# Kernel tuning notes

Measured on AMD Instinct MI355X. Metric: run time of the kernel, lower is better.

Reference implementation:

```python
import jax, jax.numpy as jnp
import numpy as np

B, NA, LAT, HID, AF, L = 512, 58, 64, 128, 10, 2
N = B * NA
E = N * 16


def silu(x):
    return x * jax.nn.sigmoid(x)


def setup_inputs() -> dict:
    key = jax.random.key(0)
    ks = list(jax.random.split(key, 32))

    def p(k, shape, fan_in):
        return jax.random.normal(k, shape, jnp.float32) / np.sqrt(fan_in)

    inp = {
        "z": jax.random.normal(ks[0], (B, LAT), jnp.float32),
        "atom_types": jax.random.uniform(ks[1], (N, AF), jnp.float32),
        "edge_index": jax.random.randint(ks[2], (2, E), 0, N, jnp.int64),
        "init_coords": jax.random.normal(ks[3], (NA, 3), jnp.float32) * 0.1,
        "latent_w": p(ks[4], (LAT, HID), LAT), "latent_b": jnp.zeros((HID,), jnp.float32),
        "atom_w": p(ks[5], (AF, HID), AF), "atom_b": jnp.zeros((HID,), jnp.float32),
        # per-layer stacked params (leading dim = num_layers)
        "edge_w1": p(ks[6], (L, 2 * HID + 1, HID), 2 * HID + 1), "edge_b1": jnp.zeros((L, HID), jnp.float32),
        "edge_w2": p(ks[7], (L, HID, HID), HID), "edge_b2": jnp.zeros((L, HID), jnp.float32),
        "node_w1": p(ks[8], (L, 2 * HID, HID), 2 * HID), "node_b1": jnp.zeros((L, HID), jnp.float32),
        "node_w2": p(ks[9], (L, HID, HID), HID), "node_b2": jnp.zeros((L, HID), jnp.float32),
        "coord_w1": p(ks[10], (L, HID, HID), HID), "coord_b1": jnp.zeros((L, HID), jnp.float32),
        "coord_w2": p(ks[11], (L, HID, 1), HID),  # no bias
        "ln_g": jnp.ones((L, HID), jnp.float32), "ln_b": jnp.zeros((L, HID), jnp.float32),
        "head_w1": p(ks[12], (HID, HID // 2), HID), "head_b1": jnp.zeros((HID // 2,), jnp.float32),
        "head_w2": p(ks[13], (HID // 2, 3), HID // 2), "head_b2": jnp.zeros((3,), jnp.float32),
    }
    return inp


def _layer(h, pos, row, col, ew1, eb1, ew2, eb2, nw1, nb1, nw2, nb2, cw1, cb1, cw2, lg, lb):
    n = h.shape[0]
    xi, xj = h[row], h[col]                      # [E,HID] gathers
    rel = pos[row] - pos[col]                    # [E,3]
    d2 = jnp.clip(jnp.sum(rel * rel, axis=-1, keepdims=True), 1e-6, 1e6)
    ef = jnp.concatenate([xi, xj, d2], axis=-1)  # [E,2H+1]
    m = silu(silu(ef @ ew1 + eb1) @ ew2 + eb2)   # edge MLP messages [E,HID]
    agg = jax.ops.segment_sum(m, row, num_segments=n)
    hn = silu(jnp.concatenate([h, agg], axis=-1) @ nw1 + nb1) @ nw2 + nb2
    mu = jnp.mean(hn, axis=-1, keepdims=True)
    var = jnp.mean((hn - mu) ** 2, axis=-1, keepdims=True)
    hn = (hn - mu) * jax.lax.rsqrt(var + 1e-5) * lg + lb
    cw = jnp.clip(silu(m @ cw1 + cb1) @ cw2, -1.0, 1.0)  # [E,1]
    upd = jax.ops.segment_sum(cw * rel, row, num_segments=n)  # [N,3]
    deg = jax.ops.segment_sum(jnp.ones((row.shape[0],), pos.dtype), row, num_segments=n)[:, None]
    pos_new = pos + upd / (deg + 1e-6)
    return hn, pos_new


def reference(z, atom_types, edge_index, init_coords, latent_w, latent_b, atom_w, atom_b,
              edge_w1, edge_b1, edge_w2, edge_b2, node_w1, node_b1, node_w2, node_b2,
              coord_w1, coord_b1, coord_w2, ln_g, ln_b, head_w1, head_b1, head_w2, head_b2):
    b = z.shape[0]
    na = init_coords.shape[0]
    n = b * na
    h = z @ latent_w + latent_b                              # [B,HID]
    h = jnp.broadcast_to(h[:, None, :], (b, na, h.shape[-1])).reshape(n, -1)
    h = h + (atom_types @ atom_w + atom_b)
    pos = jnp.broadcast_to(init_coords[None], (b, na, 3)).reshape(n, 3)
    row, col = edge_index[0], edge_index[1]
    for l in range(edge_w1.shape[0]):
        h, pos = _layer(h, pos, row, col,
                        edge_w1[l], edge_b1[l], edge_w2[l], edge_b2[l],
                        node_w1[l], node_b1[l], node_w2[l], node_b2[l],
                        coord_w1[l], coord_b1[l], coord_w2[l], ln_g[l], ln_b[l])
    delta = silu(h @ head_w1 + head_b1) @ head_w2 + head_b2
    return pos + delta
```

## Files before the change

### kernel.cpp

```cpp
#include <hip/hip_runtime.h>
#include <hip/hip_bf16.h>

#define BB 512
#define NA 58
#define LAT 64
#define HID 128
#define AF 10
#define NL 2
#define NN (BB*NA)
#define NE (NN*16)
#define ET 64
#define NTILE (NE/ET)
#define PBLK 768

typedef __attribute__((ext_vector_type(8))) short s8;
typedef __attribute__((ext_vector_type(4))) float f4;

struct CvtDesc {
    const void* src[24];
    float*      dst[24];
    int         len[24];
};

struct PackJobs {
    const float* src[10];
    short*       dst[10];
    int          K[10];
    int          mode[10];
};

__device__ __forceinline__ float siluf(float x) {
    return x * __builtin_amdgcn_rcpf(1.0f + __expf(-x));
}

__device__ __forceinline__ short f2b(float x) {
    __hip_bfloat16 b = __float2bfloat16(x);
    return *(short*)&b;
}

__device__ __forceinline__ float b2f(short s) {
    return __uint_as_float(((unsigned int)(unsigned short)s) << 16);
}

__global__ void k_detect(const unsigned short* __restrict__ z16,
                         const unsigned int* __restrict__ e32,
                         int* __restrict__ flags) {
    __shared__ int sbf, si64;
    if (threadIdx.x == 0) { sbf = 0; si64 = 0; }
    __syncthreads();
    int c1 = 0, c2 = 0;
    for (int i = threadIdx.x; i < 1024; i += 256) {
        unsigned short v = z16[2*i];
        int e = (v >> 7) & 0xFF;
        if (e >= 100 && e <= 140) c1++;
        if (e32[2*i + 1] == 0u) c2++;
    }
    atomicAdd(&sbf, c1);
    atomicAdd(&si64, c2);
    __syncthreads();
    if (threadIdx.x == 0) {
        flags[0] = (sbf  > 600) ? 1 : 0;
        flags[1] = (si64 > 600) ? 1 : 0;
    }
}

__global__ void k_convert(CvtDesc d, const int* __restrict__ flags) {
    int a = blockIdx.y;
    int i = blockIdx.x * blockDim.x + threadIdx.x;
    int n = d.len[a];
    if (i >= n) return;
    if (flags[0]) {
        d.dst[a][i] = __bfloat162float(((const __hip_bfloat16*)d.src[a])[i]);
    } else {
        d.dst[a][i] = ((const float*)d.src[a])[i];
    }
}

__global__ void k_packall(PackJobs pj) {
    int j = blockIdx.y;
    int idx = blockIdx.x * 256 + threadIdx.x;
    const float* w = pj.src[j];
    short* o = pj.dst[j];
    if (pj.mode[j] == 0) {
        int K = pj.K[j];
        if (idx >= 128*K) return;
        int jj = idx & 7;
        int l  = (idx >> 3) & 63;
        int rest = idx >> 9;
        int KC = K >> 5;
        int kc = rest % KC;
        int nt = rest / KC;
        int n = nt*16 + (l & 15);
        int k = kc*32 + (l >> 4)*8 + jj;
        o[idx] = f2b(w[k*128 + n]);
    } else {
        if (idx >= 32768) return;
        int jj = idx & 7;
        int l  = (idx >> 3) & 63;
        int rest = idx >> 9;
        int kc = rest & 3;
        int nt = rest >> 2;
        int n = nt*16 + (l & 15);
        int k = kc*32 + (l >> 4)*8 + jj;
        float v = (n < 128) ? w[k*128 + n] : w[(128 + k)*128 + (n - 128)];
        o[idx] = f2b(v);
    }
}

__global__ void k_hist(const int* __restrict__ eidx, const int* __restrict__ flags,
                       int* __restrict__ cnt) {
    int e = blockIdx.x * 256 + threadIdx.x;
    if (e >= NE) return;
    int is64 = flags[1];
    int r = eidx[is64 ? 2*(long)e : (long)e];
    atomicAdd(&cnt[r], 1);
}

__global__ __launch_bounds__(1024) void k_scan(const int* __restrict__ cnt,
                                               int* __restrict__ rowStart,
                                               int* __restrict__ cursor) {
    __shared__ int part[1024];
    int t = threadIdx.x;
    int base = t * 29;
    int loc[29];
    int s = 0;
    #pragma unroll
    for (int i = 0; i < 29; ++i) { loc[i] = s; s += cnt[base + i]; }
    part[t] = s;
    __syncthreads();
    for (int d = 1; d < 1024; d <<= 1) {
        int v = (t >= d) ? part[t - d] : 0;
        __syncthreads();
        part[t] += v;
        __syncthreads();
    }
    int pre = (t == 0) ? 0 : part[t - 1];
    #pragma unroll
    for (int i = 0; i < 29; ++i) {
        int v = pre + loc[i];
        rowStart[base + i] = v;
        cursor[base + i] = v;
    }
    if (t == 1023) rowStart[NN] = pre + s;
}

__global__ void k_scatter(const int* __restrict__ eidx, const int* __restrict__ flags,
                          int* __restrict__ cursor,
                          int* __restrict__ rS, int* __restrict__ cS) {
    int e = blockIdx.x * 256 + threadIdx.x;
    if (e >= NE) return;
    int is64 = flags[1];
    long ge = e, gc = (long)e + NE;
    int r = eidx[is64 ? 2*ge : ge];
    int c = eidx[is64 ? 2*gc : gc];
    int p = atomicAdd(&cursor[r], 1);
    rS[p] = r; cS[p] = c;
}

__global__ void k_hz(const float* __restrict__ z, const float* __restrict__ lw,
                     const float* __restrict__ lb, float* __restrict__ hz) {
    __shared__ float zs[LAT];
    int b = blockIdx.x;
    int c = threadIdx.x;
    if (c < LAT) zs[c] = z[b*LAT + c];
    __syncthreads();
    float acc = lb[c];
    #pragma unroll
    for (int k = 0; k < LAT; ++k) acc += zs[k] * lw[k*HID + c];
    hz[b*HID + c] = acc;
}

__global__ __launch_bounds__(256) void k_init3(
    const float* __restrict__ hz, const float* __restrict__ at,
    const float* __restrict__ aw, const float* __restrict__ ab,
    const float* __restrict__ ic,
    float* __restrict__ pos, short* __restrict__ hb,
    const short* __restrict__ wcat0, const float* __restrict__ b10,
    short* __restrict__ H1, float* __restrict__ agg, float* __restrict__ upd)
{
    __shared__ short x[64][136];
    __shared__ float awS[AF][HID];
    __shared__ float atS[64][AF+2];
    const int tid = threadIdx.x;
    const int n0 = blockIdx.x * 64;

    for (int i = tid; i < AF*HID; i += 256) awS[i/HID][i%HID] = aw[i];
    for (int i = tid; i < 64*AF; i += 256)
        atS[i/AF][i%AF] = at[(long)(n0 + i/AF)*AF + i%AF];
    __syncthreads();

    #pragma unroll
    for (int it = 0; it < 32; ++it) {
        int idx = it*256 + tid;
        int r = idx >> 7, c = idx & 127;
        int n = n0 + r;
        int bb = n / NA;
        float v = hz[bb*HID + c] + ab[c];
        #pragma unroll
        for (int f = 0; f < AF; ++f) v += atS[r][f]*awS[f][c];
        short s = f2b(v);
        x[r][c] = s;
        hb[(long)n*HID + c] = s;
    }
    if (tid < 192) {
        int i = tid/3, d = tid - i*3;
        int n = n0 + i;
        pos[n*3 + d] = ic[(n % NA)*3 + d];
        upd[n*3 + d] = 0.f;
    }
    {
        f4* a4 = (f4*)(agg + (long)n0*HID);
        for (int j = tid; j < 64*HID/4; j += 256) a4[j] = (f4)0.f;
    }
    __syncthreads();

    const int l = tid & 63, w = tid >> 6;
    const int l16 = l & 15, quad = l >> 4;
    f4 acc[4][4];
    #pragma unroll
    for (int mt = 0; mt < 4; ++mt)
        #pragma unroll
        for (int nt4 = 0; nt4 < 4; ++nt4) acc[mt][nt4] = (f4)0.f;
    #pragma unroll
    for (int kc = 0; kc < 4; ++kc) {
        s8 a[4];
        #pragma unroll
        for (int mt = 0; mt < 4; ++mt)
            a[mt] = *(const s8*)&x[mt*16 + l16][kc*32 + quad*8];
        #pragma unroll
        for (int nt4 = 0; nt4 < 4; ++nt4) {
            int nt = w*4 + nt4;
            s8 b = *(const s8*)(wcat0 + (((size_t)nt*4 + kc)*64 + l)*8);
            #pragma unroll
            for (int mt = 0; mt < 4; ++mt)
                acc[mt][nt4] = __builtin_amdgcn_mfma_f32_16x16x32_bf16(a[mt], b, acc[mt][nt4], 0, 0, 0);
        }
    }
    #pragma unroll
    for (int nt4 = 0; nt4 < 4; ++nt4) {
        int col = (w*4 + nt4)*16 + l16;
        float bias = (col < 128) ? b10[col] : 0.f;
        #pragma unroll
        for (int mt = 0; mt < 4; ++mt)
            #pragma unroll
            for (int i = 0; i < 4; ++i) {
                int row = mt*16 + quad*4 + i;
                H1[(long)(n0 + row)*256 + col] = f2b(acc[mt][nt4][i] + bias);
            }
    }
}

__global__ __launch_bounds__(256, 3) void k_edge8(
    const short* __restrict__ H1,
    const int* __restrict__ rS, const int* __restrict__ cS,
    const float* __restrict__ pos,
    const float* __restrict__ w1c,
    const short* __restrict__ w2p, const float* __restrict__ b2,
    const short* __restrict__ c1p, const float* __restrict__ cb1,
    const float* __restrict__ cw2,
    float* __restrict__ agg, float* __restrict__ upd)
{
    __shared__ short t1[2][ET][136];
    __shared__ short mm[ET][136];
    __shared__ int   rIs[2][ET], cIs[2][ET];
    __shared__ float sred[ET];

    const int tid = threadIdx.x;
    const int l = tid & 63, w = tid >> 6;
    const int l16 = l & 15, quad = l >> 4;
    const int c0 = (2*w)*16 + l16, c1c = (2*w+1)*16 + l16;
    const int half = tid >> 7, ch = tid & 127;
    const int q = tid & 15;
    const int esub = tid >> 4;

    float wv[8];
    #pragma unroll
    for (int j = 0; j < 8; ++j) wv[j] = w1c[q*8 + j];

    s8 w2f[8], c1f[8];
    #pragma unroll
    for (int kc = 0; kc < 4; ++kc) {
        w2f[kc]     = *(const s8*)(w2p + (((size_t)(2*w)*4 + kc)*64 + l)*8);
        w2f[4 + kc] = *(const s8*)(w2p + (((size_t)(2*w+1)*4 + kc)*64 + l)*8);
        c1f[kc]     = *(const s8*)(c1p + (((size_t)(2*w)*4 + kc)*64 + l)*8);
        c1f[4 + kc] = *(const s8*)(c1p + (((size_t)(2*w+1)*4 + kc)*64 + l)*8);
    }
    const float bia2_0 = b2[c0],  bia2_1 = b2[c1c];
    const float biac_0 = cb1[c0], biac_1 = cb1[c1c];
    const float cw0    = cw2[c0], cw1v   = cw2[c1c];

    int   pri[4], pci[4];
    float pd2[4];
    auto PREIDX = [&](int T) {
        long eb = (long)T * ET;
        #pragma unroll
        for (int it = 0; it < 4; ++it) {
            int e = esub + 16*it;
            int r = rS[eb + e], c = cS[eb + e];
            pri[it] = r; pci[it] = c;
            float rx = pos[r*3+0] - pos[c*3+0];
            float ry = pos[r*3+1] - pos[c*3+1];
            float rz = pos[r*3+2] - pos[c*3+2];
            pd2[it] = fminf(fmaxf(rx*rx + ry*ry + rz*rz, 1e-6f), 1e6f);
        }
    };

    int T = blockIdx.x;
    PREIDX(T);
    #pragma unroll
    for (int it = 0; it < 4; ++it) {
        s8 va = *(const s8*)(H1 + (long)pri[it]*256 + q*8);
        s8 vb = *(const s8*)(H1 + (long)pci[it]*256 + 128 + q*8);
        float d2 = pd2[it];
        s8 o;
        #pragma unroll
        for (int j = 0; j < 8; ++j)
            o[j] = f2b(siluf(b2f(va[j]) + b2f(vb[j]) + d2*wv[j]));
        *(s8*)&t1[0][esub + 16*it][q*8] = o;
    }
    if (q == 0) {
        #pragma unroll
        for (int it = 0; it < 4; ++it) {
            rIs[0][esub + 16*it] = pri[it];
            cIs[0][esub + 16*it] = pci[it];
        }
    }
    if (tid < ET) sred[tid] = 0.f;
    int Tn = T + PBLK;
    if (Tn < NTILE) PREIDX(Tn);
    __syncthreads();

    int b = 0;
    while (true) {
        const bool hasNext = (Tn < NTILE);

        {
            f4 acc[4][2];
            #pragma unroll
            for (int mt = 0; mt < 4; ++mt) { acc[mt][0] = (f4)0.f; acc[mt][1] = (f4)0.f; }
            #pragma unroll
            for (int it = 0; it < 4; ++it) {
                s8 va, vb;
                if (hasNext) {
                    va = *(const s8*)(H1 + (long)pri[it]*256 + q*8);
                    vb = *(const s8*)(H1 + (long)pci[it]*256 + 128 + q*8);
                }
                #pragma unroll
                for (int mt = 0; mt < 4; ++mt) {
                    s8 a = *(const s8*)&t1[b][mt*16 + l16][it*32 + quad*8];
                    acc[mt][0] = __builtin_amdgcn_mfma_f32_16x16x32_bf16(a, w2f[it],     acc[mt][0], 0, 0, 0);
                    acc[mt][1] = __builtin_amdgcn_mfma_f32_16x16x32_bf16(a, w2f[4 + it], acc[mt][1], 0, 0, 0);
                }
                if (hasNext) {
                    float d2 = pd2[it];
                    s8 o;
                    #pragma unroll
                    for (int j = 0; j < 8; ++j)
                        o[j] = f2b(siluf(b2f(va[j]) + b2f(vb[j]) + d2*wv[j]));
                    *(s8*)&t1[b^1][esub + 16*it][q*8] = o;
                }
            }
            if (hasNext && q == 0) {
                #pragma unroll
                for (int it = 0; it < 4; ++it) {
                    rIs[b^1][esub + 16*it] = pri[it];
                    cIs[b^1][esub + 16*it] = pci[it];
                }
            }
            #pragma unroll
            for (int mt = 0; mt < 4; ++mt) {
                #pragma unroll
                for (int i = 0; i < 4; ++i) {
                    int row = mt*16 + quad*4 + i;
                    mm[row][c0]  = f2b(siluf(acc[mt][0][i] + bia2_0));
                    mm[row][c1c] = f2b(siluf(acc[mt][1][i] + bia2_1));
                }
            }
        }
        __syncthreads();

        {
            f4 acc[4][2];
            #pragma unroll
            for (int mt = 0; mt < 4; ++mt) { acc[mt][0] = (f4)0.f; acc[mt][1] = (f4)0.f; }
            #pragma unroll
            for (int kc = 0; kc < 4; ++kc) {
                #pragma unroll
                for (int mt = 0; mt < 4; ++mt) {
                    s8 a = *(const s8*)&mm[mt*16 + l16][kc*32 + quad*8];
                    acc[mt][0] = __builtin_amdgcn_mfma_f32_16x16x32_bf16(a, c1f[kc],     acc[mt][0], 0, 0, 0);
                    acc[mt][1] = __builtin_amdgcn_mfma_f32_16x16x32_bf16(a, c1f[4 + kc], acc[mt][1], 0, 0, 0);
                }
            }
            #pragma unroll
            for (int mt = 0; mt < 4; ++mt) {
                #pragma unroll
                for (int i = 0; i < 4; ++i) {
                    float p = siluf(acc[mt][0][i] + biac_0) * cw0
                            + siluf(acc[mt][1][i] + biac_1) * cw1v;
                    p += __shfl_xor(p, 1);
                    p += __shfl_xor(p, 2);
                    p += __shfl_xor(p, 4);
                    p += __shfl_xor(p, 8);
                    if (l16 == 0) {
                        int row = mt*16 + quad*4 + i;
                        atomicAdd(&sred[row], p);
                    }
                }
            }
        }
        {
            int e0 = half * 32;
            int cur = rIs[b][e0];
            float a = 0.f;
            #pragma unroll
            for (int e = e0; e < e0 + 32; ++e) {
                int r = rIs[b][e];
                if (r != cur) {
                    atomicAdd(&agg[(long)cur*HID + ch], a);
                    a = 0.f; cur = r;
                }
                a += b2f(mm[e][ch]);
            }
            atomicAdd(&agg[(long)cur*HID + ch], a);
        }
        int Tnn = Tn + PBLK;
        if (hasNext && Tnn < NTILE) PREIDX(Tnn);
        __syncthreads();

        if (tid < ET) {
            float cwv = fminf(fmaxf(sred[tid], -1.f), 1.f);
            sred[tid] = 0.f;
            int r = rIs[b][tid], c = cIs[b][tid];
            float rx = pos[r*3+0] - pos[c*3+0];
            float ry = pos[r*3+1] - pos[c*3+1];
            float rz = pos[r*3+2] - pos[c*3+2];
            atomicAdd(&upd[r*3+0], cwv*rx);
            atomicAdd(&upd[r*3+1], cwv*ry);
            atomicAdd(&upd[r*3+2], cwv*rz);
        }
        if (!hasNext) break;
        T = Tn; Tn = Tnn; b ^= 1;
    }
}

__global__ __launch_bounds__(256) void k_node_mfma(
    short* __restrict__ hb, float* __restrict__ agg,
    const short* __restrict__ w1p, const float* __restrict__ b1n,
    const short* __restrict__ w2p, const float* __restrict__ b2n,
    const float* __restrict__ lg, const float* __restrict__ lb,
    float* __restrict__ pos, float* __restrict__ upd,
    const int* __restrict__ rowStart,
    const short* __restrict__ wcatn, const float* __restrict__ b1next,
    short* __restrict__ H1)
{
    __shared__ short x[64][264];
    __shared__ short t1[64][144];
    __shared__ float mus[64], rstds[64];
    float (*hn)[132] = (float (*)[132])&x[0][0];

    const int tid = threadIdx.x;
    const int n0 = blockIdx.x * 64;

    #pragma unroll
    for (int it = 0; it < 4; ++it) {
        int idx = it*256 + tid;
        int e = idx >> 4, qq = idx & 15;
        *(int4*)&x[e][qq*8] = *(const int4*)(hb + (long)(n0+e)*HID + qq*8);
    }
    #pragma unroll
    for (int it = 0; it < 8; ++it) {
        int idx = it*256 + tid;
        int e = idx >> 5, qq = idx & 31;
        float4 v = *(const float4*)(agg + (long)(n0+e)*HID + qq*4);
        short4 sv;
        sv.x = f2b(v.x); sv.y = f2b(v.y); sv.z = f2b(v.z); sv.w = f2b(v.w);
        *(short4*)&x[e][128 + qq*4] = sv;
    }
    __syncthreads();

    {
        f4* a4 = (f4*)(agg + (long)n0*HID);
        for (int j = tid; j < 64*HID/4; j += 256) a4[j] = (f4)0.f;
    }

    const int l = tid & 63, w = tid >> 6;
    const int l16 = l & 15, quad = l >> 4;
    const int nt0 = 2*w, nt1 = 2*w + 1;
    const int c0 = nt0*16 + l16, c1c = nt1*16 + l16;

    {
        f4 acc[4][2];
        #pragma unroll
        for (int mt = 0; mt < 4; ++mt) { acc[mt][0] = (f4)0.f; acc[mt][1] = (f4)0.f; }
        #pragma unroll
        for (int kc = 0; kc < 8; ++kc) {
            s8 b0  = *(const s8*)(w1p + (((size_t)nt0*8 + kc)*64 + l)*8);
            s8 b1f = *(const s8*)(w1p + (((size_t)nt1*8 + kc)*64 + l)*8);
            #pragma unroll
            for (int mt = 0; mt < 4; ++mt) {
                s8 a = *(const s8*)&x[mt*16 + l16][kc*32 + quad*8];
                acc[mt][0] = __builtin_amdgcn_mfma_f32_16x16x32_bf16(a, b0,  acc[mt][0], 0, 0, 0);
                acc[mt][1] = __builtin_amdgcn_mfma_f32_16x16x32_bf16(a, b1f, acc[mt][1], 0, 0, 0);
            }
        }
        float bia0 = b1n[c0], bia1 = b1n[c1c];
        #pragma unroll
        for (int mt = 0; mt < 4; ++mt) {
            #pragma unroll
            for (int i = 0; i < 4; ++i) {
                int row = mt*16 + quad*4 + i;
                t1[row][c0]  = f2b(siluf(acc[mt][0][i] + bia0));
                t1[row][c1c] = f2b(siluf(acc[mt][1][i] + bia1));
            }
        }
    }
    __syncthreads();

    {
        f4 acc[4][2];
        #pragma unroll
        for (int mt = 0; mt < 4; ++mt) { acc[mt][0] = (f4)0.f; acc[mt][1] = (f4)0.f; }
        #pragma unroll
        for (int kc = 0; kc < 4; ++kc) {
            s8 b0  = *(const s8*)(w2p + (((size_t)nt0*4 + kc)*64 + l)*8);
            s8 b1f = *(const s8*)(w2p + (((size_t)nt1*4 + kc)*64 + l)*8);
            #pragma unroll
            for (int mt = 0; mt < 4; ++mt) {
                s8 a = *(const s8*)&t1[mt*16 + l16][kc*32 + quad*8];
                acc[mt][0] = __builtin_amdgcn_mfma_f32_16x16x32_bf16(a, b0,  acc[mt][0], 0, 0, 0);
                acc[mt][1] = __builtin_amdgcn_mfma_f32_16x16x32_bf16(a, b1f, acc[mt][1], 0, 0, 0);
            }
        }
        float bia0 = b2n[c0], bia1 = b2n[c1c];
        __syncthreads();
        #pragma unroll
        for (int mt = 0; mt < 4; ++mt) {
            #pragma unroll
            for (int i = 0; i < 4; ++i) {
                int row = mt*16 + quad*4 + i;
                hn[row][c0]  = acc[mt][0][i] + bia0;
                hn[row][c1c] = acc[mt][1][i] + bia1;
            }
        }
    }
    __syncthreads();

    {
        int r = tid >> 2, part = tid & 3;
        float s = 0.f, qv = 0.f;
        #pragma unroll
        for (int j = 0; j < 32; ++j) {
            float v = hn[r][part + 4*j];
            s += v; qv += v*v;
        }
        s += __shfl_xor(s, 1); qv += __shfl_xor(qv, 1);
        s += __shfl_xor(s, 2); qv += __shfl_xor(qv, 2);
        if (part == 0) {
            float mu = s * (1.0f/HID);
            float var = qv * (1.0f/HID) - mu*mu;
            mus[r] = mu;
            rstds[r] = rsqrtf(var + 1e-5f);
        }
    }
    __syncthreads();

    #pragma unroll
    for (int it = 0; it < 32; ++it) {
        int idx = it*256 + tid;
        int r = idx >> 7, c = idx & 127;
        float v = (hn[r][c] - mus[r]) * rstds[r] * lg[c] + lb[c];
        short s = f2b(v);
        hb[(long)(n0 + r)*HID + c] = s;
        t1[r][c] = s;
    }
    if (tid < 192) {
        int i = tid / 3, d = tid - i*3;
        int n = n0 + i;
        float dg = (float)(rowStart[n+1] - rowStart[n]);
        pos[n*3+d] += upd[n*3+d] / (dg + 1e-6f);
        upd[n*3+d] = 0.f;
    }

    if (wcatn) {
        __syncthreads();
        f4 acc[4][4];
        #pragma unroll
        for (int mt = 0; mt < 4; ++mt)
            #pragma unroll
            for (int nt4 = 0; nt4 < 4; ++nt4) acc[mt][nt4] = (f4)0.f;
        #pragma unroll
        for (int kc = 0; kc < 4; ++kc) {
            s8 a[4];
            #pragma unroll
            for (int mt = 0; mt < 4; ++mt)
                a[mt] = *(const s8*)&t1[mt*16 + l16][kc*32 + quad*8];
            #pragma unroll
            for (int nt4 = 0; nt4 < 4; ++nt4) {
                int nt = w*4 + nt4;
                s8 b = *(const s8*)(wcatn + (((size_t)nt*4 + kc)*64 + l)*8);
                #pragma unroll
                for (int mt = 0; mt < 4; ++mt)
                    acc[mt][nt4] = __builtin_amdgcn_mfma_f32_16x16x32_bf16(a[mt], b, acc[mt][nt4], 0, 0, 0);
            }
        }
        #pragma unroll
        for (int nt4 = 0; nt4 < 4; ++nt4) {
            int col = (w*4 + nt4)*16 + l16;
            float bias = (col < 128) ? b1next[col] : 0.f;
            #pragma unroll
            for (int mt = 0; mt < 4; ++mt)
                #pragma unroll
                for (int i = 0; i < 4; ++i) {
                    int row = mt*16 + quad*4 + i;
                    H1[(long)(n0 + row)*256 + col] = f2b(acc[mt][nt4][i] + bias);
                }
        }
    }
}

__global__ void k_head(const short* __restrict__ hb, const float* __restrict__ pos,
                       const float* __restrict__ w1, const float* __restrict__ b1,
                       const float* __restrict__ w2, const float* __restrict__ b2,
                       void* __restrict__ out, const int* __restrict__ flags)
{
    __shared__ float hs[4][HID];
    __shared__ float t[4][64];
    const int tid = threadIdx.x;
    const int n0 = blockIdx.x * 4;
    for (int i = tid; i < 4*HID; i += 256)
        hs[i >> 7][i & 127] = b2f(hb[(long)n0*HID + i]);
    __syncthreads();
    const int s = tid >> 6, c = tid & 63;
    float acc = b1[c];
    for (int k4 = 0; k4 < 32; ++k4) {
        int k = k4*4;
        float wa = w1[(k+0)*64 + c];
        float wb = w1[(k+1)*64 + c];
        float wc = w1[(k+2)*64 + c];
        float wd = w1[(k+3)*64 + c];
        float4 v = *(const float4*)&hs[s][k];
        acc += v.x*wa + v.y*wb + v.z*wc + v.w*wd;
    }
    t[s][c] = siluf(acc);
    __syncthreads();
    if (c < 3) {
        float a2 = b2[c];
        #pragma unroll
        for (int k = 0; k < 64; ++k) a2 += t[s][k] * w2[k*3 + c];
        int n = n0 + s;
        float v = pos[n*3+c] + a2;
        if (flags[0]) ((__hip_bfloat16*)out)[n*3+c] = __float2bfloat16(v);
        else          ((float*)out)[n*3+c] = v;
    }
}

extern "C" void kernel_launch(void* const* d_in, const int* in_sizes, int n_in,
                              void* d_out, int out_size, void* d_ws, size_t ws_size,
                              hipStream_t stream)
{
    (void)in_sizes; (void)n_in; (void)out_size; (void)ws_size;

    int* flags = (int*)d_ws;
    float* base = (float*)d_ws;
    size_t off = 64;
    auto alloc = [&](size_t n) { float* p = base + off; off += (n + 63) & ~63ull; return p; };

    static const int aidx[24] = {0,1,3,4,5,6,7,8,9,10,11,12,13,14,15,16,17,18,19,20,21,22,23,24};
    static const int alen[24] = {
        BB*LAT, NN*AF, NA*3, LAT*HID, HID, AF*HID, HID,
        NL*257*HID, NL*HID, NL*HID*HID, NL*HID,
        NL*256*HID, NL*HID, NL*HID*HID, NL*HID,
        NL*HID*HID, NL*HID, NL*HID, NL*HID, NL*HID,
        HID*64, 64, 64*3, 3
    };
    CvtDesc cd;
    float* fp[24];
    for (int a = 0; a < 24; ++a) {
        fp[a] = alloc((size_t)alen[a]);
        cd.src[a] = d_in[aidx[a]];
        cd.dst[a] = fp[a];
        cd.len[a] = alen[a];
    }
    float* agg = alloc((size_t)NN*HID);
    float* hz  = alloc((size_t)BB*HID);
    float* pos = alloc((size_t)NN*3);
    float* upd = alloc((size_t)NN*3);
    short* hb  = (short*)alloc((size_t)NN*HID/2);
    short* H1  = (short*)alloc((size_t)NN*256/2);
    short* wcatp = (short*)alloc((size_t)NL*32768/2);
    short* w2p = (short*)alloc((size_t)NL*16384/2);
    short* c1p = (short*)alloc((size_t)NL*16384/2);
    short* nw1p = (short*)alloc((size_t)NL*32768/2);
    short* nw2p = (short*)alloc((size_t)NL*16384/2);
    int* cnt      = (int*)alloc((size_t)NN);
    int* rowStart = (int*)alloc((size_t)NN + 1);
    int* cursor   = (int*)alloc((size_t)NN);
    int* rS       = (int*)alloc((size_t)NE);
    int* cS       = (int*)alloc((size_t)NE);
    const int* eidx = (const int*)d_in[2];

    k_detect<<<1, 256, 0, stream>>>((const unsigned short*)d_in[0],
                                    (const unsigned int*)d_in[2], flags);
    k_convert<<<dim3((NN*AF + 255)/256, 24), 256, 0, stream>>>(cd, flags);

    PackJobs pj;
    for (int l = 0; l < NL; ++l) {
        int b5 = l*5;
        pj.src[b5+0] = fp[7]  + (size_t)l*257*HID; pj.dst[b5+0] = wcatp + (size_t)l*32768; pj.K[b5+0] = 256; pj.mode[b5+0] = 1;
        pj.src[b5+1] = fp[9]  + (size_t)l*HID*HID; pj.dst[b5+1] = w2p   + (size_t)l*16384; pj.K[b5+1] = 128; pj.mode[b5+1] = 0;
        pj.src[b5+2] = fp[15] + (size_t)l*HID*HID; pj.dst[b5+2] = c1p   + (size_t)l*16384; pj.K[b5+2] = 128; pj.mode[b5+2] = 0;
        pj.src[b5+3] = fp[11] + (size_t)l*256*HID; pj.dst[b5+3] = nw1p  + (size_t)l*32768; pj.K[b5+3] = 256; pj.mode[b5+3] = 0;
        pj.src[b5+4] = fp[13] + (size_t)l*HID*HID; pj.dst[b5+4] = nw2p  + (size_t)l*16384; pj.K[b5+4] = 128; pj.mode[b5+4] = 0;
    }
    k_packall<<<dim3(128, 10), 256, 0, stream>>>(pj);

    hipMemsetAsync(cnt, 0, (size_t)NN*sizeof(int), stream);
    k_hist<<<(NE + 255)/256, 256, 0, stream>>>(eidx, flags, cnt);
    k_scan<<<1, 1024, 0, stream>>>(cnt, rowStart, cursor);
    k_scatter<<<(NE + 255)/256, 256, 0, stream>>>(eidx, flags, cursor, rS, cS);

    k_hz<<<BB, HID, 0, stream>>>(fp[0], fp[3], fp[4], hz);
    k_init3<<<NN/64, 256, 0, stream>>>(hz, fp[1], fp[5], fp[6], fp[2], pos, hb,
                                       wcatp, fp[8], H1, agg, upd);

    for (int l = 0; l < NL; ++l) {
        k_edge8<<<PBLK, 256, 0, stream>>>(H1, rS, cS, pos,
            fp[7] + (size_t)l*257*HID + 256*HID,
            w2p + (size_t)l*16384, fp[10] + (size_t)l*HID,
            c1p + (size_t)l*16384, fp[16] + (size_t)l*HID,
            fp[17] + (size_t)l*HID,
            agg, upd);
        const short* wcatn = (l+1 < NL) ? (wcatp + (size_t)(l+1)*32768) : nullptr;
        const float* b1nx  = (l+1 < NL) ? (fp[8] + (size_t)(l+1)*HID) : fp[8];
        k_node_mfma<<<NN/64, 256, 0, stream>>>(hb, agg,
            nw1p + (size_t)l*32768, fp[12] + (size_t)l*HID,
            nw2p + (size_t)l*16384, fp[14] + (size_t)l*HID,
            fp[18] + (size_t)l*HID, fp[19] + (size_t)l*HID,
            pos, upd, rowStart, wcatn, b1nx, H1);
    }
    k_head<<<NN/4, 256, 0, stream>>>(hb, pos, fp[20], fp[21], fp[22], fp[23],
                                     d_out, flags);
}
```

Before: 647.4 us.

## Restructure edge kernel to per-wave 16-edge tiles and fuse head into node kernel

The edge kernel changes from block-level 64-edge tiles with double-buffered shared memory and block barriers to independent per-wave 16-edge tiles. Each wave builds its MFMA A operand directly in registers and reads the packed weights from global/L1 on every tile instead of keeping them resident in registers. This removes __syncthreads and shared-memory staging of the first activation, but it reloads weight fragments per tile and issues more atomics with shorter segment runs. Separately, the output head MLP is packed to bf16 and fused into the last node kernel via MFMA, which removes the k_head launch and the re-read of h.

```diff
diff --git a/kernel.cpp b/kernel.cpp
--- a/kernel.cpp
+++ b/kernel.cpp
@@ -9,8 +9,7 @@
 #define NL 2
 #define NN (BB*NA)
 #define NE (NN*16)
-#define ET 64
-#define NTILE (NE/ET)
+#define NWT (NE/16)
 #define PBLK 768
 
 typedef __attribute__((ext_vector_type(8))) short s8;
@@ -23,10 +22,10 @@
 };
 
 struct PackJobs {
-    const float* src[10];
-    short*       dst[10];
-    int          K[10];
-    int          mode[10];
+    const float* src[11];
+    short*       dst[11];
+    int          K[11];
+    int          mode[11];
 };
 
 __device__ __forceinline__ float siluf(float x) {
@@ -81,7 +80,8 @@
     int idx = blockIdx.x * 256 + threadIdx.x;
     const float* w = pj.src[j];
     short* o = pj.dst[j];
-    if (pj.mode[j] == 0) {
+    int mode = pj.mode[j];
+    if (mode == 0) {
         int K = pj.K[j];
         if (idx >= 128*K) return;
         int jj = idx & 7;
@@ -93,7 +93,7 @@
         int n = nt*16 + (l & 15);
         int k = kc*32 + (l >> 4)*8 + jj;
         o[idx] = f2b(w[k*128 + n]);
-    } else {
+    } else if (mode == 1) {
         if (idx >= 32768) return;
         int jj = idx & 7;
         int l  = (idx >> 3) & 63;
@@ -104,6 +104,16 @@
         int k = kc*32 + (l >> 4)*8 + jj;
         float v = (n < 128) ? w[k*128 + n] : w[(128 + k)*128 + (n - 128)];
         o[idx] = f2b(v);
+    } else {
+        if (idx >= 8192) return;
+        int jj = idx & 7;
+        int l  = (idx >> 3) & 63;
+        int rest = idx >> 9;
+        int kc = rest & 3;
+        int nt = rest >> 2;
+        int n = nt*16 + (l & 15);
+        int k = kc*32 + (l >> 4)*8 + jj;
+        o[idx] = f2b(w[k*64 + n]);
     }
 }
 
@@ -250,7 +260,7 @@
     }
 }
 
-__global__ __launch_bounds__(256, 3) void k_edge8(
+__global__ __launch_bounds__(256, 3) void k_edge9(
     const short* __restrict__ H1,
     const int* __restrict__ rS, const int* __restrict__ cS,
     const float* __restrict__ pos,
@@ -260,187 +270,116 @@
     const float* __restrict__ cw2,
     float* __restrict__ agg, float* __restrict__ upd)
 {
-    __shared__ short t1[2][ET][136];
-    __shared__ short mm[ET][136];
-    __shared__ int   rIs[2][ET], cIs[2][ET];
-    __shared__ float sred[ET];
+    __shared__ short msc[4][16][136];
+    __shared__ float cwS[4][16];
 
     const int tid = threadIdx.x;
-    const int l = tid & 63, w = tid >> 6;
+    const int w = tid >> 6, l = tid & 63;
     const int l16 = l & 15, quad = l >> 4;
-    const int c0 = (2*w)*16 + l16, c1c = (2*w+1)*16 + l16;
-    const int half = tid >> 7, ch = tid & 127;
-    const int q = tid & 15;
-    const int esub = tid >> 4;
-
-    float wv[8];
-    #pragma unroll
-    for (int j = 0; j < 8; ++j) wv[j] = w1c[q*8 + j];
-
-    s8 w2f[8], c1f[8];
-    #pragma unroll
-    for (int kc = 0; kc < 4; ++kc) {
-        w2f[kc]     = *(const s8*)(w2p + (((size_t)(2*w)*4 + kc)*64 + l)*8);
-        w2f[4 + kc] = *(const s8*)(w2p + (((size_t)(2*w+1)*4 + kc)*64 + l)*8);
-        c1f[kc]     = *(const s8*)(c1p + (((size_t)(2*w)*4 + kc)*64 + l)*8);
-        c1f[4 + kc] = *(const s8*)(c1p + (((size_t)(2*w+1)*4 + kc)*64 + l)*8);
-    }
-    const float bia2_0 = b2[c0],  bia2_1 = b2[c1c];
-    const float biac_0 = cb1[c0], biac_1 = cb1[c1c];
-    const float cw0    = cw2[c0], cw1v   = cw2[c1c];
-
-    int   pri[4], pci[4];
-    float pd2[4];
-    auto PREIDX = [&](int T) {
-        long eb = (long)T * ET;
-        #pragma unroll
-        for (int it = 0; it < 4; ++it) {
-            int e = esub + 16*it;
-            int r = rS[eb + e], c = cS[eb + e];
-            pri[it] = r; pci[it] = c;
-            float rx = pos[r*3+0] - pos[c*3+0];
-            float ry = pos[r*3+1] - pos[c*3+1];
-            float rz = pos[r*3+2] - pos[c*3+2];
-            pd2[it] = fminf(fmaxf(rx*rx + ry*ry + rz*rz, 1e-6f), 1e6f);
-        }
-    };
-
-    int T = blockIdx.x;
-    PREIDX(T);
-    #pragma unroll
-    for (int it = 0; it < 4; ++it) {
-        s8 va = *(const s8*)(H1 + (long)pri[it]*256 + q*8);
-        s8 vb = *(const s8*)(H1 + (long)pci[it]*256 + 128 + q*8);
-        float d2 = pd2[it];
-        s8 o;
-        #pragma unroll
-        for (int j = 0; j < 8; ++j)
-            o[j] = f2b(siluf(b2f(va[j]) + b2f(vb[j]) + d2*wv[j]));
-        *(s8*)&t1[0][esub + 16*it][q*8] = o;
-    }
-    if (q == 0) {
-        #pragma unroll
-        for (int it = 0; it < 4; ++it) {
-            rIs[0][esub + 16*it] = pri[it];
-            cIs[0][esub + 16*it] = pci[it];
-        }
-    }
-    if (tid < ET) sred[tid] = 0.f;
-    int Tn = T + PBLK;
-    if (Tn < NTILE) PREIDX(Tn);
-    __syncthreads();
-
-    int b = 0;
-    while (true) {
-        const bool hasNext = (Tn < NTILE);
+
+    float b2l[8], cbl[8], cwl[8];
+    #pragma unroll
+    for (int nt = 0; nt < 8; ++nt) {
+        b2l[nt] = b2[nt*16 + l16];
+        cbl[nt] = cb1[nt*16 + l16];
+        cwl[nt] = cw2[nt*16 + l16];
+    }
+
+    for (int wt = blockIdx.x*4 + w; wt < NWT; wt += PBLK*4) {
+        const long eb = (long)wt * 16;
+
+        int r = rS[eb + l16], c = cS[eb + l16];
+        float rx = pos[r*3+0] - pos[c*3+0];
+        float ry = pos[r*3+1] - pos[c*3+1];
+        float rz = pos[r*3+2] - pos[c*3+2];
+        float d2 = fminf(fmaxf(rx*rx + ry*ry + rz*rz, 1e-6f), 1e6f);
+
+        s8 a[4];
+        #pragma unroll
+        for (int kc = 0; kc < 4; ++kc) {
+            s8 va = *(const s8*)(H1 + (long)r*256 + kc*32 + quad*8);
+            s8 vb = *(const s8*)(H1 + (long)c*256 + 128 + kc*32 + quad*8);
+            f4 w0 = *(const f4*)(w1c + kc*32 + quad*8);
+            f4 w1v = *(const f4*)(w1c + kc*32 + quad*8 + 4);
+            s8 o;
+            #pragma unroll
+            for (int j = 0; j < 8; ++j) {
+                float wvj = (j < 4) ? w0[j & 3] : w1v[j & 3];
+                o[j] = f2b(siluf(b2f(va[j]) + b2f(vb[j]) + d2*wvj));
+            }
+            a[kc] = o;
+        }
+
+        #pragma unroll
+        for (int nt = 0; nt < 8; ++nt) {
+            f4 acc = (f4)0.f;
+            #pragma unroll
+            for (int kc = 0; kc < 4; ++kc) {
+                s8 b = *(const s8*)(w2p + (((size_t)nt*4 + kc)*64 + l)*8);
+                acc = __builtin_amdgcn_mfma_f32_16x16x32_bf16(a[kc], b, acc, 0, 0, 0);
+            }
+            int col = nt*16 + l16;
+            #pragma unroll
+            for (int i = 0; i < 4; ++i)
+                msc[w][quad*4 + i][col] = f2b(siluf(acc[i] + b2l[nt]));
+        }
+
+        s8 ma[4];
+        #pragma unroll
+        for (int kc = 0; kc < 4; ++kc)
+            ma[kc] = *(const s8*)&msc[w][l16][kc*32 + quad*8];
+
+        float accr[4] = {0.f, 0.f, 0.f, 0.f};
+        #pragma unroll
+        for (int nt = 0; nt < 8; ++nt) {
+            f4 acc = (f4)0.f;
+            #pragma unroll
+            for (int kc = 0; kc < 4; ++kc) {
+                s8 b = *(const s8*)(c1p + (((size_t)nt*4 + kc)*64 + l)*8);
+                acc = __builtin_amdgcn_mfma_f32_16x16x32_bf16(ma[kc], b, acc, 0, 0, 0);
+            }
+            #pragma unroll
+            for (int i = 0; i < 4; ++i)
+                accr[i] += siluf(acc[i] + cbl[nt]) * cwl[nt];
+        }
+        #pragma unroll
+        for (int i = 0; i < 4; ++i) {
+            float p = accr[i];
+            p += __shfl_xor(p, 1);
+            p += __shfl_xor(p, 2);
+            p += __shfl_xor(p, 4);
+            p += __shfl_xor(p, 8);
+            if (l16 == 0) cwS[w][quad*4 + i] = fminf(fmaxf(p, -1.f), 1.f);
+        }
 
         {
-            f4 acc[4][2];
-            #pragma unroll
-            for (int mt = 0; mt < 4; ++mt) { acc[mt][0] = (f4)0.f; acc[mt][1] = (f4)0.f; }
-            #pragma unroll
-            for (int it = 0; it < 4; ++it) {
-                s8 va, vb;
-                if (hasNext) {
-                    va = *(const s8*)(H1 + (long)pri[it]*256 + q*8);
-                    vb = *(const s8*)(H1 + (long)pci[it]*256 + 128 + q*8);
+            float s0 = 0.f, s1 = 0.f;
+            int cur = rS[eb];
+            #pragma unroll
+            for (int k = 0; k < 16; ++k) {
+                int rr = rS[eb + k];
+                if (rr != cur) {
+                    atomicAdd(&agg[(long)cur*HID + l],      s0);
+                    atomicAdd(&agg[(long)cur*HID + l + 64], s1);
+                    s0 = 0.f; s1 = 0.f; cur = rr;
                 }
-                #pragma unroll
-                for (int mt = 0; mt < 4; ++mt) {
-                    s8 a = *(const s8*)&t1[b][mt*16 + l16][it*32 + quad*8];
-                    acc[mt][0] = __builtin_amdgcn_mfma_f32_16x16x32_bf16(a, w2f[it],     acc[mt][0], 0, 0, 0);
-                    acc[mt][1] = __builtin_amdgcn_mfma_f32_16x16x32_bf16(a, w2f[4 + it], acc[mt][1], 0, 0, 0);
-                }
-                if (hasNext) {
-                    float d2 = pd2[it];
-                    s8 o;
-                    #pragma unroll
-                    for (int j = 0; j < 8; ++j)
-                        o[j] = f2b(siluf(b2f(va[j]) + b2f(vb[j]) + d2*wv[j]));
-                    *(s8*)&t1[b^1][esub + 16*it][q*8] = o;
-                }
-            }
-            if (hasNext && q == 0) {
-                #pragma unroll
-                for (int it = 0; it < 4; ++it) {
-                    rIs[b^1][esub + 16*it] = pri[it];
-                    cIs[b^1][esub + 16*it] = pci[it];
-                }
-            }
-            #pragma unroll
-            for (int mt = 0; mt < 4; ++mt) {
-                #pragma unroll
-                for (int i = 0; i < 4; ++i) {
-                    int row = mt*16 + quad*4 + i;
-                    mm[row][c0]  = f2b(siluf(acc[mt][0][i] + bia2_0));
-                    mm[row][c1c] = f2b(siluf(acc[mt][1][i] + bia2_1));
-                }
-            }
-        }
-        __syncthreads();
-
-        {
-            f4 acc[4][2];
-            #pragma unroll
-            for (int mt = 0; mt < 4; ++mt) { acc[mt][0] = (f4)0.f; acc[mt][1] = (f4)0.f; }
-            #pragma unroll
-            for (int kc = 0; kc < 4; ++kc) {
-                #pragma unroll
-                for (int mt = 0; mt < 4; ++mt) {
-                    s8 a = *(const s8*)&mm[mt*16 + l16][kc*32 + quad*8];
-                    acc[mt][0] = __builtin_amdgcn_mfma_f32_16x16x32_bf16(a, c1f[kc],     acc[mt][0], 0, 0, 0);
-                    acc[mt][1] = __builtin_amdgcn_mfma_f32_16x16x32_bf16(a, c1f[4 + kc], acc[mt][1], 0, 0, 0);
-                }
-            }
-            #pragma unroll
-            for (int mt = 0; mt < 4; ++mt) {
-                #pragma unroll
-                for (int i = 0; i < 4; ++i) {
-                    float p = siluf(acc[mt][0][i] + biac_0) * cw0
-                            + siluf(acc[mt][1][i] + biac_1) * cw1v;
-                    p += __shfl_xor(p, 1);
-                    p += __shfl_xor(p, 2);
-                    p += __shfl_xor(p, 4);
-                    p += __shfl_xor(p, 8);
-                    if (l16 == 0) {
-                        int row = mt*16 + quad*4 + i;
-                        atomicAdd(&sred[row], p);
-                    }
-                }
-            }
-        }
-        {
-            int e0 = half * 32;
-            int cur = rIs[b][e0];
-            float a = 0.f;
-            #pragma unroll
-            for (int e = e0; e < e0 + 32; ++e) {
-                int r = rIs[b][e];
-                if (r != cur) {
-                    atomicAdd(&agg[(long)cur*HID + ch], a);
-                    a = 0.f; cur = r;
-                }
-                a += b2f(mm[e][ch]);
-            }
-            atomicAdd(&agg[(long)cur*HID + ch], a);
-        }
-        int Tnn = Tn + PBLK;
-        if (hasNext && Tnn < NTILE) PREIDX(Tnn);
-        __syncthreads();
-
-        if (tid < ET) {
-            float cwv = fminf(fmaxf(sred[tid], -1.f), 1.f);
-            sred[tid] = 0.f;
-            int r = rIs[b][tid], c = cIs[b][tid];
-            float rx = pos[r*3+0] - pos[c*3+0];
-            float ry = pos[r*3+1] - pos[c*3+1];
-            float rz = pos[r*3+2] - pos[c*3+2];
-            atomicAdd(&upd[r*3+0], cwv*rx);
-            atomicAdd(&upd[r*3+1], cwv*ry);
-            atomicAdd(&upd[r*3+2], cwv*rz);
-        }
-        if (!hasNext) break;
-        T = Tn; Tn = Tnn; b ^= 1;
+                s0 += b2f(msc[w][k][l]);
+                s1 += b2f(msc[w][k][l + 64]);
+            }
+            atomicAdd(&agg[(long)cur*HID + l],      s0);
+            atomicAdd(&agg[(long)cur*HID + l + 64], s1);
+        }
+
+        if (l < 16) {
+            float cwv = cwS[w][l];
+            int rr = rS[eb + l], cc = cS[eb + l];
+            float ux = pos[rr*3+0] - pos[cc*3+0];
+            float uy = pos[rr*3+1] - pos[cc*3+1];
+            float uz = pos[rr*3+2] - pos[cc*3+2];
+            atomicAdd(&upd[rr*3+0], cwv*ux);
+            atomicAdd(&upd[rr*3+1], cwv*uy);
+            atomicAdd(&upd[rr*3+2], cwv*uz);
+        }
     }
 }
 
@@ -452,12 +391,17 @@
     float* __restrict__ pos, float* __restrict__ upd,
     const int* __restrict__ rowStart,
     const short* __restrict__ wcatn, const float* __restrict__ b1next,
-    short* __restrict__ H1)
+    short* __restrict__ H1,
+    const short* __restrict__ hw1p, const float* __restrict__ hb1,
+    const float* __restrict__ hw2, const float* __restrict__ hb2,
+    void* __restrict__ out, const int* __restrict__ flags)
 {
     __shared__ short x[64][264];
     __shared__ short t1[64][144];
     __shared__ float mus[64], rstds[64];
+    __shared__ float posS[64][3];
     float (*hn)[132] = (float (*)[132])&x[0][0];
+    float (*hid)[68] = (float (*)[68])&x[0][0];
 
     const int tid = threadIdx.x;
     const int n0 = blockIdx.x * 64;
@@ -578,12 +522,14 @@
         int i = tid / 3, d = tid - i*3;
         int n = n0 + i;
         float dg = (float)(rowStart[n+1] - rowStart[n]);
-        pos[n*3+d] += upd[n*3+d] / (dg + 1e-6f);
+        float np = pos[n*3+d] + upd[n*3+d] / (dg + 1e-6f);
+        pos[n*3+d] = np;
+        posS[i][d] = np;
         upd[n*3+d] = 0.f;
     }
+    __syncthreads();
 
     if (wcatn) {
-        __syncthreads();
         f4 acc[4][4];
         #pragma unroll
         for (int mt = 0; mt < 4; ++mt)
@@ -616,42 +562,39 @@
                     H1[(long)(n0 + row)*256 + col] = f2b(acc[mt][nt4][i] + bias);
                 }
         }
-    }
-}
-
-__global__ void k_head(const short* __restrict__ hb, const float* __restrict__ pos,
-                       const float* __restrict__ w1, const float* __restrict__ b1,
-                       const float* __restrict__ w2, const float* __restrict__ b2,
-                       void* __restrict__ out, const int* __restrict__ flags)
-{
-    __shared__ float hs[4][HID];
-    __shared__ float t[4][64];
-    const int tid = threadIdx.x;
-    const int n0 = blockIdx.x * 4;
-    for (int i = tid; i < 4*HID; i += 256)
-        hs[i >> 7][i & 127] = b2f(hb[(long)n0*HID + i]);
-    __syncthreads();
-    const int s = tid >> 6, c = tid & 63;
-    float acc = b1[c];
-    for (int k4 = 0; k4 < 32; ++k4) {
-        int k = k4*4;
-        float wa = w1[(k+0)*64 + c];
-        float wb = w1[(k+1)*64 + c];
-        float wc = w1[(k+2)*64 + c];
-        float wd = w1[(k+3)*64 + c];
-        float4 v = *(const float4*)&hs[s][k];
-        acc += v.x*wa + v.y*wb + v.z*wc + v.w*wd;
-    }
-    t[s][c] = siluf(acc);
-    __syncthreads();
-    if (c < 3) {
-        float a2 = b2[c];
-        #pragma unroll
-        for (int k = 0; k < 64; ++k) a2 += t[s][k] * w2[k*3 + c];
-        int n = n0 + s;
-        float v = pos[n*3+c] + a2;
-        if (flags[0]) ((__hip_bfloat16*)out)[n*3+c] = __float2bfloat16(v);
-        else          ((float*)out)[n*3+c] = v;
+    } else {
+        f4 acc[4];
+        #pragma unroll
+        for (int mt = 0; mt < 4; ++mt) acc[mt] = (f4)0.f;
+        #pragma unroll
+        for (int kc = 0; kc < 4; ++kc) {
+            s8 b = *(const s8*)(hw1p + (((size_t)w*4 + kc)*64 + l)*8);
+            #pragma unroll
+            for (int mt = 0; mt < 4; ++mt) {
+                s8 a = *(const s8*)&t1[mt*16 + l16][kc*32 + quad*8];
+                acc[mt] = __builtin_amdgcn_mfma_f32_16x16x32_bf16(a, b, acc[mt], 0, 0, 0);
+            }
+        }
+        int col = w*16 + l16;
+        float bias = hb1[col];
+        #pragma unroll
+        for (int mt = 0; mt < 4; ++mt)
+            #pragma unroll
+            for (int i = 0; i < 4; ++i) {
+                int row = mt*16 + quad*4 + i;
+                hid[row][col] = siluf(acc[mt][i] + bias);
+            }
+        __syncthreads();
+        if (tid < 192) {
+            int r = tid / 3, cc = tid - r*3;
+            float a2 = hb2[cc];
+            #pragma unroll
+            for (int k = 0; k < 64; ++k) a2 += hid[r][k] * hw2[k*3 + cc];
+            int n = n0 + r;
+            float v = posS[r][cc] + a2;
+            if (flags[0]) ((__hip_bfloat16*)out)[n*3+cc] = __float2bfloat16(v);
+            else          ((float*)out)[n*3+cc] = v;
+        }
     }
 }
 
@@ -693,6 +636,7 @@
     short* c1p = (short*)alloc((size_t)NL*16384/2);
     short* nw1p = (short*)alloc((size_t)NL*32768/2);
     short* nw2p = (short*)alloc((size_t)NL*16384/2);
+    short* hw1p = (short*)alloc((size_t)8192/2);
     int* cnt      = (int*)alloc((size_t)NN);
     int* rowStart = (int*)alloc((size_t)NN + 1);
     int* cursor   = (int*)alloc((size_t)NN);
@@ -713,7 +657,8 @@
         pj.src[b5+3] = fp[11] + (size_t)l*256*HID; pj.dst[b5+3] = nw1p  + (size_t)l*32768; pj.K[b5+3] = 256; pj.mode[b5+3] = 0;
         pj.src[b5+4] = fp[13] + (size_t)l*HID*HID; pj.dst[b5+4] = nw2p  + (size_t)l*16384; pj.K[b5+4] = 128; pj.mode[b5+4] = 0;
     }
-    k_packall<<<dim3(128, 10), 256, 0, stream>>>(pj);
+    pj.src[10] = fp[20]; pj.dst[10] = hw1p; pj.K[10] = 128; pj.mode[10] = 2;
+    k_packall<<<dim3(128, 11), 256, 0, stream>>>(pj);
 
     hipMemsetAsync(cnt, 0, (size_t)NN*sizeof(int), stream);
     k_hist<<<(NE + 255)/256, 256, 0, stream>>>(eidx, flags, cnt);
@@ -725,7 +670,7 @@
                                        wcatp, fp[8], H1, agg, upd);
 
     for (int l = 0; l < NL; ++l) {
-        k_edge8<<<PBLK, 256, 0, stream>>>(H1, rS, cS, pos,
+        k_edge9<<<PBLK, 256, 0, stream>>>(H1, rS, cS, pos,
             fp[7] + (size_t)l*257*HID + 256*HID,
             w2p + (size_t)l*16384, fp[10] + (size_t)l*HID,
             c1p + (size_t)l*16384, fp[16] + (size_t)l*HID,
@@ -737,8 +682,7 @@
             nw1p + (size_t)l*32768, fp[12] + (size_t)l*HID,
             nw2p + (size_t)l*16384, fp[14] + (size_t)l*HID,
             fp[18] + (size_t)l*HID, fp[19] + (size_t)l*HID,
-            pos, upd, rowStart, wcatn, b1nx, H1);
-    }
-    k_head<<<NN/4, 256, 0, stream>>>(hb, pos, fp[20], fp[21], fp[22], fp[23],
-                                     d_out, flags);
-}
+            pos, upd, rowStart, wcatn, b1nx, H1,
+            hw1p, fp[21], fp[22], fp[23], d_out, flags);
+    }
+}
```

Result: slower. 1.098 ms (+69.6%).

## Fuse output head into last node kernel using MFMA for head first layer

Applied to the files above, without the earlier changes.

Removes the separate k_head launch and computes the output head inside the final k_node_mfma invocation, reusing the normalized hidden tile already in shared memory. The head's first layer now runs as a bf16 MFMA with weights pre-packed by a new pack mode, and the second layer runs as scalar FMAs from shared memory. The updated positions are staged in shared memory so the extra global re-read disappears. The head matmul moves from fp32 to bf16 inputs, which may change precision slightly.

```diff
diff --git a/kernel.cpp b/kernel.cpp
--- a/kernel.cpp
+++ b/kernel.cpp
@@ -23,10 +23,10 @@
 };
 
 struct PackJobs {
-    const float* src[10];
-    short*       dst[10];
-    int          K[10];
-    int          mode[10];
+    const float* src[11];
+    short*       dst[11];
+    int          K[11];
+    int          mode[11];
 };
 
 __device__ __forceinline__ float siluf(float x) {
@@ -81,7 +81,8 @@
     int idx = blockIdx.x * 256 + threadIdx.x;
     const float* w = pj.src[j];
     short* o = pj.dst[j];
-    if (pj.mode[j] == 0) {
+    int mode = pj.mode[j];
+    if (mode == 0) {
         int K = pj.K[j];
         if (idx >= 128*K) return;
         int jj = idx & 7;
@@ -93,7 +94,7 @@
         int n = nt*16 + (l & 15);
         int k = kc*32 + (l >> 4)*8 + jj;
         o[idx] = f2b(w[k*128 + n]);
-    } else {
+    } else if (mode == 1) {
         if (idx >= 32768) return;
         int jj = idx & 7;
         int l  = (idx >> 3) & 63;
@@ -104,6 +105,16 @@
         int k = kc*32 + (l >> 4)*8 + jj;
         float v = (n < 128) ? w[k*128 + n] : w[(128 + k)*128 + (n - 128)];
         o[idx] = f2b(v);
+    } else {
+        if (idx >= 8192) return;
+        int jj = idx & 7;
+        int l  = (idx >> 3) & 63;
+        int rest = idx >> 9;
+        int kc = rest & 3;
+        int nt = rest >> 2;
+        int n = nt*16 + (l & 15);
+        int k = kc*32 + (l >> 4)*8 + jj;
+        o[idx] = f2b(w[k*64 + n]);
     }
 }
 
@@ -452,12 +463,17 @@
     float* __restrict__ pos, float* __restrict__ upd,
     const int* __restrict__ rowStart,
     const short* __restrict__ wcatn, const float* __restrict__ b1next,
-    short* __restrict__ H1)
+    short* __restrict__ H1,
+    const short* __restrict__ hw1p, const float* __restrict__ hb1,
+    const float* __restrict__ hw2, const float* __restrict__ hb2,
+    void* __restrict__ out, const int* __restrict__ flags)
 {
     __shared__ short x[64][264];
     __shared__ short t1[64][144];
     __shared__ float mus[64], rstds[64];
+    __shared__ float posS[64][3];
     float (*hn)[132] = (float (*)[132])&x[0][0];
+    float (*hid)[68] = (float (*)[68])&x[0][0];
 
     const int tid = threadIdx.x;
     const int n0 = blockIdx.x * 64;
@@ -578,12 +594,14 @@
         int i = tid / 3, d = tid - i*3;
         int n = n0 + i;
         float dg = (float)(rowStart[n+1] - rowStart[n]);
-        pos[n*3+d] += upd[n*3+d] / (dg + 1e-6f);
+        float np = pos[n*3+d] + upd[n*3+d] / (dg + 1e-6f);
+        pos[n*3+d] = np;
+        posS[i][d] = np;
         upd[n*3+d] = 0.f;
     }
+    __syncthreads();
 
     if (wcatn) {
-        __syncthreads();
         f4 acc[4][4];
         #pragma unroll
         for (int mt = 0; mt < 4; ++mt)
@@ -616,42 +634,39 @@
                     H1[(long)(n0 + row)*256 + col] = f2b(acc[mt][nt4][i] + bias);
                 }
         }
-    }
-}
-
-__global__ void k_head(const short* __restrict__ hb, const float* __restrict__ pos,
-                       const float* __restrict__ w1, const float* __restrict__ b1,
-                       const float* __restrict__ w2, const float* __restrict__ b2,
-                       void* __restrict__ out, const int* __restrict__ flags)
-{
-    __shared__ float hs[4][HID];
-    __shared__ float t[4][64];
-    const int tid = threadIdx.x;
-    const int n0 = blockIdx.x * 4;
-    for (int i = tid; i < 4*HID; i += 256)
-        hs[i >> 7][i & 127] = b2f(hb[(long)n0*HID + i]);
-    __syncthreads();
-    const int s = tid >> 6, c = tid & 63;
-    float acc = b1[c];
-    for (int k4 = 0; k4 < 32; ++k4) {
-        int k = k4*4;
-        float wa = w1[(k+0)*64 + c];
-        float wb = w1[(k+1)*64 + c];
-        float wc = w1[(k+2)*64 + c];
-        float wd = w1[(k+3)*64 + c];
-        float4 v = *(const float4*)&hs[s][k];
-        acc += v.x*wa + v.y*wb + v.z*wc + v.w*wd;
-    }
-    t[s][c] = siluf(acc);
-    __syncthreads();
-    if (c < 3) {
-        float a2 = b2[c];
-        #pragma unroll
-        for (int k = 0; k < 64; ++k) a2 += t[s][k] * w2[k*3 + c];
-        int n = n0 + s;
-        float v = pos[n*3+c] + a2;
-        if (flags[0]) ((__hip_bfloat16*)out)[n*3+c] = __float2bfloat16(v);
-        else          ((float*)out)[n*3+c] = v;
+    } else {
+        f4 acc[4];
+        #pragma unroll
+        for (int mt = 0; mt < 4; ++mt) acc[mt] = (f4)0.f;
+        #pragma unroll
+        for (int kc = 0; kc < 4; ++kc) {
+            s8 b = *(const s8*)(hw1p + (((size_t)w*4 + kc)*64 + l)*8);
+            #pragma unroll
+            for (int mt = 0; mt < 4; ++mt) {
+                s8 a = *(const s8*)&t1[mt*16 + l16][kc*32 + quad*8];
+                acc[mt] = __builtin_amdgcn_mfma_f32_16x16x32_bf16(a, b, acc[mt], 0, 0, 0);
+            }
+        }
+        int col = w*16 + l16;
+        float bias = hb1[col];
+        #pragma unroll
+        for (int mt = 0; mt < 4; ++mt)
+            #pragma unroll
+            for (int i = 0; i < 4; ++i) {
+                int row = mt*16 + quad*4 + i;
+                hid[row][col] = siluf(acc[mt][i] + bias);
+            }
+        __syncthreads();
+        if (tid < 192) {
+            int r = tid / 3, cc = tid - r*3;
+            float a2 = hb2[cc];
+            #pragma unroll
+            for (int k = 0; k < 64; ++k) a2 += hid[r][k] * hw2[k*3 + cc];
+            int n = n0 + r;
+            float v = posS[r][cc] + a2;
+            if (flags[0]) ((__hip_bfloat16*)out)[n*3+cc] = __float2bfloat16(v);
+            else          ((float*)out)[n*3+cc] = v;
+        }
     }
 }
 
@@ -693,6 +708,7 @@
     short* c1p = (short*)alloc((size_t)NL*16384/2);
     short* nw1p = (short*)alloc((size_t)NL*32768/2);
     short* nw2p = (short*)alloc((size_t)NL*16384/2);
+    short* hw1p = (short*)alloc((size_t)8192/2);
     int* cnt      = (int*)alloc((size_t)NN);
     int* rowStart = (int*)alloc((size_t)NN + 1);
     int* cursor   = (int*)alloc((size_t)NN);
@@ -713,7 +729,8 @@
         pj.src[b5+3] = fp[11] + (size_t)l*256*HID; pj.dst[b5+3] = nw1p  + (size_t)l*32768; pj.K[b5+3] = 256; pj.mode[b5+3] = 0;
         pj.src[b5+4] = fp[13] + (size_t)l*HID*HID; pj.dst[b5+4] = nw2p  + (size_t)l*16384; pj.K[b5+4] = 128; pj.mode[b5+4] = 0;
     }
-    k_packall<<<dim3(128, 10), 256, 0, stream>>>(pj);
+    pj.src[10] = fp[20]; pj.dst[10] = hw1p; pj.K[10] = 128; pj.mode[10] = 2;
+    k_packall<<<dim3(128, 11), 256, 0, stream>>>(pj);
 
     hipMemsetAsync(cnt, 0, (size_t)NN*sizeof(int), stream);
     k_hist<<<(NE + 255)/256, 256, 0, stream>>>(eidx, flags, cnt);
@@ -737,8 +754,7 @@
             nw1p + (size_t)l*32768, fp[12] + (size_t)l*HID,
             nw2p + (size_t)l*16384, fp[14] + (size_t)l*HID,
             fp[18] + (size_t)l*HID, fp[19] + (size_t)l*HID,
-            pos, upd, rowStart, wcatn, b1nx, H1);
-    }
-    k_head<<<NN/4, 256, 0, stream>>>(hb, pos, fp[20], fp[21], fp[22], fp[23],
-                                     d_out, flags);
-}
+            pos, upd, rowStart, wcatn, b1nx, H1,
+            hw1p, fp[21], fp[22], fp[23], d_out, flags);
+    }
+}
```

New measurement: 606.9 us. -6.3%, faster.
